# Kernel tuning notes

Hardware: AMD Instinct MI355X
Metric: run time of the kernel (lower is better)

The kernel has to match this reference:

```python
import jax, jax.numpy as jnp
import numpy as np

B = 256   # batch (bs)
N = 6890  # SMPL vertices
J = 24    # joints (root + 23)
NB = 10   # betas
P = 100   # points per foot plane
PARENTS = np.array([-1,0,0,0,1,2,3,4,5,6,7,8,9,9,9,12,13,14,16,17,18,19,20,21], dtype=np.int64)


def setup_inputs() -> dict:
    key = jax.random.key(0)
    ks = jax.random.split(key, 20)
    v_template = jax.random.normal(ks[0], (N, 3), jnp.float32) * 0.3
    shapedirs = jax.random.normal(ks[1], (N, 3, NB), jnp.float32) * 0.01
    Jr = jax.random.uniform(ks[2], (J, N), jnp.float32)
    J_regressor = Jr / Jr.sum(axis=1, keepdims=True)
    lw = jax.random.uniform(ks[3], (N, J), jnp.float32)
    lbs_weights = lw / lw.sum(axis=1, keepdims=True)
    betas = jnp.concatenate([jnp.ones((1, 1), jnp.float32),
                             jax.random.normal(ks[4], (1, NB), jnp.float32) * 0.5], axis=1)
    return dict(
        v_template=v_template, shapedirs=shapedirs, J_regressor=J_regressor,
        lbs_weights=lbs_weights, betas=betas,
        body_pose_wo_foot=jax.random.normal(ks[5], (B, 57), jnp.float32) * 0.2,
        r_back_foot_pose=jax.random.normal(ks[6], (B, 3), jnp.float32) * 0.2,
        r_front_foot_pose=jax.random.normal(ks[7], (B,), jnp.float32) * 0.2,
        l_back_foot_pose=jax.random.normal(ks[8], (B, 3), jnp.float32) * 0.2,
        l_front_foot_pose=jax.random.normal(ks[9], (B,), jnp.float32) * 0.2,
        transl=jax.random.normal(ks[10], (B, 3), jnp.float32) * 0.1,
        global_orient=jax.random.normal(ks[11], (B, 3), jnp.float32) * 0.2,
        init_plane_back_l=jax.random.normal(ks[12], (B, P, 3), jnp.float32) * 0.1,
        init_plane_front_l=jax.random.normal(ks[13], (B, P, 3), jnp.float32) * 0.1,
        init_plane_back_r=jax.random.normal(ks[14], (B, P, 3), jnp.float32) * 0.1,
        init_plane_front_r=jax.random.normal(ks[15], (B, P, 3), jnp.float32) * 0.1,
        parents=jnp.asarray(PARENTS),
        foot_back_l_ids=jax.random.randint(ks[16], (P,), 0, N),
        foot_back_r_ids=jax.random.randint(ks[17], (P,), 0, N),
        foot_front_l_ids=jax.random.randint(ks[18], (P,), 0, N),
        foot_front_r_ids=jax.random.randint(ks[19], (P,), 0, N),
    )


def _rodrigues(rot_vecs):
    # rot_vecs: [M,3] axis-angle -> [M,3,3] rotation matrices (matches SMPL batch_rodrigues)
    angle = jnp.linalg.norm(rot_vecs + 1e-8, axis=1, keepdims=True)  # [M,1]
    rot_dir = rot_vecs / angle
    cos = jnp.cos(angle)[..., None]  # [M,1,1]
    sin = jnp.sin(angle)[..., None]
    rx, ry, rz = rot_dir[:, 0], rot_dir[:, 1], rot_dir[:, 2]
    zeros = jnp.zeros_like(rx)
    K = jnp.stack([zeros, -rz, ry, rz, zeros, -rx, -ry, rx, zeros], axis=1).reshape(-1, 3, 3)
    I = jnp.eye(3, dtype=rot_vecs.dtype)
    return I + sin * K + (1.0 - cos) * jnp.matmul(K, K)


def _forward(v_template, shapedirs, J_regressor, lbs_weights, betas,
             body_pose_wo_foot, r_back_foot_pose, r_front_foot_pose,
             l_back_foot_pose, l_front_foot_pose, transl, global_orient,
             init_plane_back_l, init_plane_front_l, init_plane_back_r, init_plane_front_r,
             ids):
    Bn = body_pose_wo_foot.shape[0]
    dt = v_template.dtype
    # --- update_shape ---
    blend = jnp.einsum('bl,mkl->bmk', betas[:, 1:], shapedirs)            # [1,N,3]
    v_shaped = (v_template[None] + blend) * betas[:, 0][:, None, None]    # [1,N,3]
    J_shaped = jnp.einsum('bik,ji->bjk', v_shaped, J_regressor)           # [1,J,3]
    # --- assemble full pose (foot-joint splicing) ---
    z2 = jnp.zeros((Bn, 2), dt)
    body_pose = jnp.concatenate([
        body_pose_wo_foot[:, :18],              # joints 1..6
        l_back_foot_pose,                       # joint 7
        r_back_foot_pose,                       # joint 8
        body_pose_wo_foot[:, 18:21],            # joint 9
        l_front_foot_pose[:, None], z2,         # joint 10 (x only)
        r_front_foot_pose[:, None], z2,         # joint 11 (x only)
        body_pose_wo_foot[:, 21:]], axis=1)     # joints 12..23
    full_pose = jnp.concatenate([global_orient, body_pose], axis=1)      # [B,72]
    rot = _rodrigues(full_pose.reshape(-1, 3)).reshape(Bn, J, 3, 3)
    # --- batch_rigid_transform ---
    joints = jnp.broadcast_to(J_shaped, (Bn, J, 3))
    rel = jnp.concatenate([joints[:, :1], joints[:, 1:] - joints[:, PARENTS[1:]]], axis=1)
    top = jnp.concatenate([rot, rel[..., None]], axis=-1)                 # [B,J,3,4]
    bottom = jnp.broadcast_to(jnp.array([0., 0., 0., 1.], dt), (Bn, J, 1, 4))
    T_loc = jnp.concatenate([top, bottom], axis=2)                        # [B,J,4,4]
    chain = [T_loc[:, 0]]
    for i in range(1, J):  # fixed 24-joint kinematic chain
        chain.append(chain[int(PARENTS[i])] @ T_loc[:, i])
    transforms = jnp.stack(chain, axis=1)                                 # [B,J,4,4]
    J_transformed = transforms[..., :3, 3]
    init_bone = jnp.einsum('bjmn,bjn->bjm', transforms[..., :3, :3], joints)
    A = transforms.at[..., :3, 3].add(-init_bone)                         # relative transforms
    # --- LBS skinning ---
    T = jnp.einsum('vj,bjmn->bvmn', lbs_weights, A)                       # [B,N,4,4]
    verts = jnp.einsum('bvmn,vn->bvm', T[:, :, :3, :3], v_shaped[0]) + T[:, :, :3, 3] + transl[:, None]
    # --- foot planes ---
    def _plane(idx, init):
        Tp = T[:, idx]                                                    # [B,P,4,4]
        return jnp.einsum('bpmn,bpn->bpm', Tp[:, :, :3, :3], init) + Tp[:, :, :3, 3]
    bl, fl, br, fr = ids
    v_plane = jnp.concatenate([
        _plane(bl, init_plane_back_l), _plane(fl, init_plane_front_l),
        _plane(br, init_plane_back_r), _plane(fr, init_plane_front_r)], axis=1) + transl[:, None]
    return verts, J_transformed, v_plane


def reference(v_template, shapedirs, J_regressor, lbs_weights, betas,
              body_pose_wo_foot, r_back_foot_pose, r_front_foot_pose,
              l_back_foot_pose, l_front_foot_pose, transl, global_orient,
              init_plane_back_l, init_plane_front_l, init_plane_back_r, init_plane_front_r,
              parents, foot_back_l_ids, foot_back_r_ids, foot_front_l_ids, foot_front_r_ids):
    ids = (foot_back_l_ids, foot_front_l_ids, foot_back_r_ids, foot_front_r_ids)
    return _forward(v_template, shapedirs, J_regressor, lbs_weights, betas,
                    body_pose_wo_foot, r_back_foot_pose, r_front_foot_pose,
                    l_back_foot_pose, l_front_foot_pose, transl, global_orient,
                    init_plane_back_l, init_plane_front_l, init_plane_back_r, init_plane_front_r,
                    ids)
```

## Files before the change

kernel.cpp:

```cpp
#include <hip/hip_runtime.h>
#include <stdint.h>

#define NV 6890
#define NJ 24
#define NB_ 256
#define NP 100
#define NBS 8

#define O_VS 0
#define O_JS 20672
#define O_A  20800

#define OUT_JT   5291520
#define OUT_PLN  5309952

__constant__ int c_par[24] = {-1,0,0,0,1,2,3,4,5,6,7,8,9,9,9,12,13,14,16,17,18,19,20,21};

__global__ void k_vshaped(const float* __restrict__ vt, const float* __restrict__ sd,
                          const float* __restrict__ betas, float* __restrict__ ws) {
    int idx = blockIdx.x * 256 + threadIdx.x;
    if (idx >= NV * 3) return;
    float b0 = betas[0];
    float acc = vt[idx];
    const float* row = sd + (size_t)idx * 10;
#pragma unroll
    for (int l = 0; l < 10; ++l) acc += betas[1 + l] * row[l];
    ws[O_VS + idx] = acc * b0;
}

__global__ void k_jshaped(const float* __restrict__ jreg, float* __restrict__ ws) {
    int j = blockIdx.x;
    int tid = threadIdx.x;
    const float* vs = ws + O_VS;
    float s0 = 0.f, s1 = 0.f, s2 = 0.f;
    for (int i = tid; i < NV; i += 256) {
        float w = jreg[(size_t)j * NV + i];
        s0 += w * vs[3 * i + 0];
        s1 += w * vs[3 * i + 1];
        s2 += w * vs[3 * i + 2];
    }
    __shared__ float r0[256], r1[256], r2[256];
    r0[tid] = s0; r1[tid] = s1; r2[tid] = s2;
    __syncthreads();
    for (int off = 128; off > 0; off >>= 1) {
        if (tid < off) { r0[tid] += r0[tid + off]; r1[tid] += r1[tid + off]; r2[tid] += r2[tid + off]; }
        __syncthreads();
    }
    if (tid == 0) {
        ws[O_JS + j * 3 + 0] = r0[0];
        ws[O_JS + j * 3 + 1] = r1[0];
        ws[O_JS + j * 3 + 2] = r2[0];
    }
}

__global__ void k_chain(const float* __restrict__ bpwf, const float* __restrict__ rback,
                        const float* __restrict__ rfront, const float* __restrict__ lback,
                        const float* __restrict__ lfront, const float* __restrict__ gor,
                        float* __restrict__ ws, float* __restrict__ out) {
    int b = blockIdx.x;
    int j = threadIdx.x;
    const float* js = ws + O_JS;
    __shared__ float sT[24][12];
    __shared__ float sJ[24][3];
    if (j < 24) {
        float px, py, pz;
        if (j == 0)      { px = gor[b*3];   py = gor[b*3+1];   pz = gor[b*3+2]; }
        else if (j <= 6) { int o = b*57 + 3*(j-1); px = bpwf[o]; py = bpwf[o+1]; pz = bpwf[o+2]; }
        else if (j == 7) { px = lback[b*3]; py = lback[b*3+1]; pz = lback[b*3+2]; }
        else if (j == 8) { px = rback[b*3]; py = rback[b*3+1]; pz = rback[b*3+2]; }
        else if (j == 9) { int o = b*57 + 18;     px = bpwf[o]; py = bpwf[o+1]; pz = bpwf[o+2]; }
        else if (j == 10){ px = lfront[b];  py = 0.f; pz = 0.f; }
        else if (j == 11){ px = rfront[b];  py = 0.f; pz = 0.f; }
        else             { int o = b*57 + 21 + 3*(j-12); px = bpwf[o]; py = bpwf[o+1]; pz = bpwf[o+2]; }
        float ax = px + 1e-8f, ay = py + 1e-8f, az = pz + 1e-8f;
        float ang = sqrtf(ax*ax + ay*ay + az*az);
        float inv = 1.0f / ang;
        float dx = px * inv, dy = py * inv, dz = pz * inv;
        float c = cosf(ang), s = sinf(ang), t = 1.0f - c;
        sJ[j][0] = js[j*3]; sJ[j][1] = js[j*3+1]; sJ[j][2] = js[j*3+2];
        int p = c_par[j];
        float rx = sJ[j][0], ry = sJ[j][1], rz = sJ[j][2];
        if (p >= 0) { rx -= js[p*3]; ry -= js[p*3+1]; rz -= js[p*3+2]; }
        sT[j][0] = 1.f - t*(dy*dy + dz*dz);
        sT[j][1] = -s*dz + t*dx*dy;
        sT[j][2] =  s*dy + t*dx*dz;
        sT[j][3] = rx;
        sT[j][4] =  s*dz + t*dx*dy;
        sT[j][5] = 1.f - t*(dx*dx + dz*dz);
        sT[j][6] = -s*dx + t*dy*dz;
        sT[j][7] = ry;
        sT[j][8] = -s*dy + t*dx*dz;
        sT[j][9] =  s*dx + t*dy*dz;
        sT[j][10]= 1.f - t*(dx*dx + dy*dy);
        sT[j][11]= rz;
    }
    __syncthreads();
    if (j < 24) {
        int path[12]; int d = 0; int cur = j;
        while (cur >= 0) { path[d++] = cur; cur = c_par[cur]; }
        float g[12];
        int r = path[d - 1];
#pragma unroll
        for (int m = 0; m < 12; ++m) g[m] = sT[r][m];
        for (int i = d - 2; i >= 0; --i) {
            int n = path[i];
            float h[12];
#pragma unroll
            for (int row = 0; row < 3; ++row) {
                float a0 = g[row*4+0], a1 = g[row*4+1], a2 = g[row*4+2], a3 = g[row*4+3];
                h[row*4+0] = a0*sT[n][0] + a1*sT[n][4] + a2*sT[n][8];
                h[row*4+1] = a0*sT[n][1] + a1*sT[n][5] + a2*sT[n][9];
                h[row*4+2] = a0*sT[n][2] + a1*sT[n][6] + a2*sT[n][10];
                h[row*4+3] = a0*sT[n][3] + a1*sT[n][7] + a2*sT[n][11] + a3;
            }
#pragma unroll
            for (int m = 0; m < 12; ++m) g[m] = h[m];
        }
        size_t jo = (size_t)OUT_JT + ((size_t)b * 24 + j) * 3;
        out[jo+0] = g[3]; out[jo+1] = g[7]; out[jo+2] = g[11];
        float jx = sJ[j][0], jy = sJ[j][1], jz = sJ[j][2];
        float* Ab = ws + O_A + ((size_t)b * 24 + j) * 12;
        Ab[0] = g[0]; Ab[1] = g[1]; Ab[2]  = g[2];  Ab[3]  = g[3]  - (g[0]*jx + g[1]*jy + g[2]*jz);
        Ab[4] = g[4]; Ab[5] = g[5]; Ab[6]  = g[6];  Ab[7]  = g[7]  - (g[4]*jx + g[5]*jy + g[6]*jz);
        Ab[8] = g[8]; Ab[9] = g[9]; Ab[10] = g[10]; Ab[11] = g[11] - (g[8]*jx + g[9]*jy + g[10]*jz);
    }
}

__global__ __launch_bounds__(256) void k_lbs(const float* __restrict__ lw,
                                             const float* __restrict__ ws,
                                             const float* __restrict__ transl,
                                             float* __restrict__ out) {
    int v = blockIdx.x * 256 + threadIdx.x;
    if (v >= NV) return;
    float w[24];
    const float* wr = lw + (size_t)v * 24;
#pragma unroll
    for (int j = 0; j < 24; ++j) w[j] = wr[j];
    float vx = ws[O_VS + v*3 + 0], vy = ws[O_VS + v*3 + 1], vz = ws[O_VS + v*3 + 2];
    int b0 = blockIdx.y * NBS;
#pragma unroll 1
    for (int bb = 0; bb < NBS; ++bb) {
        int b = b0 + bb;
        const float* Ab = ws + O_A + (size_t)b * 288;
        float T[12];
#pragma unroll
        for (int m = 0; m < 12; ++m) T[m] = 0.f;
#pragma unroll
        for (int j = 0; j < 24; ++j) {
            float wj = w[j];
#pragma unroll
            for (int m = 0; m < 12; ++m) T[m] += wj * Ab[j*12 + m];
        }
        float ox = T[0]*vx + T[1]*vy + T[2]*vz  + T[3]  + transl[b*3+0];
        float oy = T[4]*vx + T[5]*vy + T[6]*vz  + T[7]  + transl[b*3+1];
        float oz = T[8]*vx + T[9]*vy + T[10]*vz + T[11] + transl[b*3+2];
        size_t o = ((size_t)b * NV + v) * 3;
        out[o+0] = ox; out[o+1] = oy; out[o+2] = oz;
    }
}

__global__ void k_plane(const float* __restrict__ lw, const float* __restrict__ ws,
                        const float* __restrict__ transl,
                        const int* __restrict__ ids_bl, const int* __restrict__ ids_fl,
                        const int* __restrict__ ids_br, const int* __restrict__ ids_fr,
                        const float* __restrict__ ip_bl, const float* __restrict__ ip_fl,
                        const float* __restrict__ ip_br, const float* __restrict__ ip_fr,
                        float* __restrict__ out) {
    int plane = blockIdx.x;
    int b = blockIdx.y;
    int p = threadIdx.x;
    if (p >= NP) return;
    const int* ids   = (plane == 0) ? ids_bl : (plane == 1) ? ids_fl : (plane == 2) ? ids_br : ids_fr;
    const float* ip  = (plane == 0) ? ip_bl  : (plane == 1) ? ip_fl  : (plane == 2) ? ip_br  : ip_fr;
    int vid = ids[p];
    const float* Ab = ws + O_A + (size_t)b * 288;
    const float* w = lw + (size_t)vid * 24;
    float T[12];
#pragma unroll
    for (int m = 0; m < 12; ++m) T[m] = 0.f;
#pragma unroll
    for (int j = 0; j < NJ; ++j) {
        float wj = w[j];
#pragma unroll
        for (int m = 0; m < 12; ++m) T[m] += wj * Ab[j * 12 + m];
    }
    size_t io = ((size_t)b * NP + p) * 3;
    float vx = ip[io+0], vy = ip[io+1], vz = ip[io+2];
    float ox = T[0]*vx + T[1]*vy + T[2]*vz  + T[3]  + transl[b*3+0];
    float oy = T[4]*vx + T[5]*vy + T[6]*vz  + T[7]  + transl[b*3+1];
    float oz = T[8]*vx + T[9]*vy + T[10]*vz + T[11] + transl[b*3+2];
    size_t o = (size_t)OUT_PLN + ((size_t)b * 400 + plane * 100 + p) * 3;
    out[o+0] = ox; out[o+1] = oy; out[o+2] = oz;
}

extern "C" void kernel_launch(void* const* d_in, const int* in_sizes, int n_in,
                              void* d_out, int out_size, void* d_ws, size_t ws_size,
                              hipStream_t stream) {
    const float* vt     = (const float*)d_in[0];
    const float* sd     = (const float*)d_in[1];
    const float* jreg   = (const float*)d_in[2];
    const float* lw     = (const float*)d_in[3];
    const float* betas  = (const float*)d_in[4];
    const float* bpwf   = (const float*)d_in[5];
    const float* rback  = (const float*)d_in[6];
    const float* rfront = (const float*)d_in[7];
    const float* lback  = (const float*)d_in[8];
    const float* lfront = (const float*)d_in[9];
    const float* transl = (const float*)d_in[10];
    const float* gor    = (const float*)d_in[11];
    const float* ip_bl  = (const float*)d_in[12];
    const float* ip_fl  = (const float*)d_in[13];
    const float* ip_br  = (const float*)d_in[14];
    const float* ip_fr  = (const float*)d_in[15];
    const int* ids_bl = (const int*)d_in[17];
    const int* ids_br = (const int*)d_in[18];
    const int* ids_fl = (const int*)d_in[19];
    const int* ids_fr = (const int*)d_in[20];

    float* ws  = (float*)d_ws;
    float* out = (float*)d_out;

    k_vshaped<<<dim3((NV * 3 + 255) / 256), 256, 0, stream>>>(vt, sd, betas, ws);
    k_jshaped<<<dim3(NJ), 256, 0, stream>>>(jreg, ws);
    k_chain  <<<dim3(NB_), 64, 0, stream>>>(bpwf, rback, rfront, lback, lfront, gor, ws, out);
    k_lbs    <<<dim3((NV + 255) / 256, NB_ / NBS), 256, 0, stream>>>(lw, ws, transl, out);
    k_plane  <<<dim3(4, NB_), 128, 0, stream>>>(lw, ws, transl, ids_bl, ids_fl, ids_br, ids_fr,
                                                ip_bl, ip_fl, ip_br, ip_fr, out);
}
```

Baseline: 174.7 us.

## Recast LBS skinning as bf16 MFMA GEMM and fuse launches into three kernels

Skinning is rewritten as one GEMM: a per-vertex matrix of weight times homogeneous rest vertex [6912x96] is multiplied by a per-batch transform matrix [768x96], both in bf16, on MFMA 16x16x32 instructions. The result is staged through shared memory and written out with transl added. The five kernels become three: the shape and joint-regression blocks are merged (joint regression recomputes shaped vertices itself), weight packing is merged with the kinematic chain, and the plane transform is merged into the GEMM kernel. This cuts the scalar FMA work and launch overhead, but bf16 operands lower the precision of the output vertices.

```diff
diff --git a/kernel.cpp b/kernel.cpp
--- a/kernel.cpp
+++ b/kernel.cpp
@@ -5,39 +5,68 @@
 #define NJ 24
 #define NB_ 256
 #define NP 100
-#define NBS 8
+#define MP 6912
+
+typedef unsigned short u16;
+typedef unsigned int u32;
+typedef __attribute__((ext_vector_type(8))) short bf16x8;
+typedef __attribute__((ext_vector_type(4))) float f32x4;
+
+__device__ __forceinline__ u16 f2bf(float f) {
+    u32 u = __float_as_uint(f);
+    u += 0x7FFFu + ((u >> 16) & 1u);
+    return (u16)(u >> 16);
+}
+
+__constant__ int c_par[24] = {-1,0,0,0,1,2,3,4,5,6,7,8,9,9,9,12,13,14,16,17,18,19,20,21};
 
 #define O_VS 0
 #define O_JS 20672
 #define O_A  20800
+#define O_WT 189056
+#define O_AT 852608
 
 #define OUT_JT   5291520
 #define OUT_PLN  5309952
 
-__constant__ int c_par[24] = {-1,0,0,0,1,2,3,4,5,6,7,8,9,9,9,12,13,14,16,17,18,19,20,21};
-
-__global__ void k_vshaped(const float* __restrict__ vt, const float* __restrict__ sd,
-                          const float* __restrict__ betas, float* __restrict__ ws) {
-    int idx = blockIdx.x * 256 + threadIdx.x;
-    if (idx >= NV * 3) return;
+__global__ __launch_bounds__(256) void k_shape(const float* __restrict__ vt,
+                                               const float* __restrict__ sd,
+                                               const float* __restrict__ jreg,
+                                               const float* __restrict__ betas,
+                                               float* __restrict__ ws) {
+    int bx = blockIdx.x;
     float b0 = betas[0];
-    float acc = vt[idx];
-    const float* row = sd + (size_t)idx * 10;
-#pragma unroll
-    for (int l = 0; l < 10; ++l) acc += betas[1 + l] * row[l];
-    ws[O_VS + idx] = acc * b0;
-}
-
-__global__ void k_jshaped(const float* __restrict__ jreg, float* __restrict__ ws) {
-    int j = blockIdx.x;
+    if (bx < 81) {
+        int idx = bx * 256 + threadIdx.x;
+        if (idx < NV * 3) {
+            float acc = vt[idx];
+            const float* row = sd + (size_t)idx * 10;
+#pragma unroll
+            for (int l = 0; l < 10; ++l) acc += betas[1 + l] * row[l];
+            ws[O_VS + idx] = acc * b0;
+        }
+        return;
+    }
+    int j = bx - 81;
     int tid = threadIdx.x;
-    const float* vs = ws + O_VS;
+    float be[10];
+#pragma unroll
+    for (int l = 0; l < 10; ++l) be[l] = betas[1 + l];
     float s0 = 0.f, s1 = 0.f, s2 = 0.f;
     for (int i = tid; i < NV; i += 256) {
         float w = jreg[(size_t)j * NV + i];
-        s0 += w * vs[3 * i + 0];
-        s1 += w * vs[3 * i + 1];
-        s2 += w * vs[3 * i + 2];
+        const float* sr = sd + (size_t)i * 30;
+        const float* vr = vt + (size_t)i * 3;
+        float c0 = vr[0], c1 = vr[1], c2 = vr[2];
+#pragma unroll
+        for (int l = 0; l < 10; ++l) {
+            c0 += be[l] * sr[l];
+            c1 += be[l] * sr[10 + l];
+            c2 += be[l] * sr[20 + l];
+        }
+        s0 += w * (c0 * b0);
+        s1 += w * (c1 * b0);
+        s2 += w * (c2 * b0);
     }
     __shared__ float r0[256], r1[256], r2[256];
     r0[tid] = s0; r1[tid] = s1; r2[tid] = s2;
@@ -53,11 +82,31 @@
     }
 }
 
-__global__ void k_chain(const float* __restrict__ bpwf, const float* __restrict__ rback,
-                        const float* __restrict__ rfront, const float* __restrict__ lback,
-                        const float* __restrict__ lfront, const float* __restrict__ gor,
-                        float* __restrict__ ws, float* __restrict__ out) {
-    int b = blockIdx.x;
+__global__ __launch_bounds__(256) void k_prep(const float* __restrict__ lw,
+                                              const float* __restrict__ bpwf,
+                                              const float* __restrict__ rback,
+                                              const float* __restrict__ rfront,
+                                              const float* __restrict__ lback,
+                                              const float* __restrict__ lfront,
+                                              const float* __restrict__ gor,
+                                              float* __restrict__ ws,
+                                              u16* __restrict__ wsu,
+                                              float* __restrict__ out) {
+    int bx = blockIdx.x;
+    if (bx < 2592) {
+        int idx = bx * 256 + threadIdx.x;
+        int v = idx / 96, k = idx - 96 * v;
+        u16 o = 0;
+        if (v < NV) {
+            int j = k >> 2, n = k & 3;
+            float w = lw[(size_t)v * 24 + j];
+            float h = (n < 3) ? ws[O_VS + v * 3 + n] : 1.0f;
+            o = f2bf(w * h);
+        }
+        wsu[O_WT + idx] = o;
+        return;
+    }
+    int b = bx - 2592;
     int j = threadIdx.x;
     const float* js = ws + O_JS;
     __shared__ float sT[24][12];
@@ -119,78 +168,111 @@
         size_t jo = (size_t)OUT_JT + ((size_t)b * 24 + j) * 3;
         out[jo+0] = g[3]; out[jo+1] = g[7]; out[jo+2] = g[11];
         float jx = sJ[j][0], jy = sJ[j][1], jz = sJ[j][2];
+        float Av[12];
+        Av[0]=g[0]; Av[1]=g[1]; Av[2]=g[2];   Av[3] = g[3]  - (g[0]*jx + g[1]*jy + g[2]*jz);
+        Av[4]=g[4]; Av[5]=g[5]; Av[6]=g[6];   Av[7] = g[7]  - (g[4]*jx + g[5]*jy + g[6]*jz);
+        Av[8]=g[8]; Av[9]=g[9]; Av[10]=g[10]; Av[11]= g[11] - (g[8]*jx + g[9]*jy + g[10]*jz);
         float* Ab = ws + O_A + ((size_t)b * 24 + j) * 12;
-        Ab[0] = g[0]; Ab[1] = g[1]; Ab[2]  = g[2];  Ab[3]  = g[3]  - (g[0]*jx + g[1]*jy + g[2]*jz);
-        Ab[4] = g[4]; Ab[5] = g[5]; Ab[6]  = g[6];  Ab[7]  = g[7]  - (g[4]*jx + g[5]*jy + g[6]*jz);
-        Ab[8] = g[8]; Ab[9] = g[9]; Ab[10] = g[10]; Ab[11] = g[11] - (g[8]*jx + g[9]*jy + g[10]*jz);
-    }
-}
-
-__global__ __launch_bounds__(256) void k_lbs(const float* __restrict__ lw,
-                                             const float* __restrict__ ws,
-                                             const float* __restrict__ transl,
-                                             float* __restrict__ out) {
-    int v = blockIdx.x * 256 + threadIdx.x;
-    if (v >= NV) return;
-    float w[24];
-    const float* wr = lw + (size_t)v * 24;
-#pragma unroll
-    for (int j = 0; j < 24; ++j) w[j] = wr[j];
-    float vx = ws[O_VS + v*3 + 0], vy = ws[O_VS + v*3 + 1], vz = ws[O_VS + v*3 + 2];
-    int b0 = blockIdx.y * NBS;
-#pragma unroll 1
-    for (int bb = 0; bb < NBS; ++bb) {
-        int b = b0 + bb;
+#pragma unroll
+        for (int m = 0; m < 12; ++m) Ab[m] = Av[m];
+        u16* at = wsu + O_AT;
+#pragma unroll
+        for (int m = 0; m < 3; ++m)
+#pragma unroll
+            for (int n = 0; n < 4; ++n)
+                at[(size_t)(b*3 + m) * 96 + j*4 + n] = f2bf(Av[m*4 + n]);
+    }
+}
+
+__global__ __launch_bounds__(256) void k_main(const u16* __restrict__ wsu,
+                                              const float* __restrict__ ws,
+                                              const float* __restrict__ lw,
+                                              const float* __restrict__ transl,
+                                              const int* __restrict__ ids_bl,
+                                              const int* __restrict__ ids_fl,
+                                              const int* __restrict__ ids_br,
+                                              const int* __restrict__ ids_fr,
+                                              const float* __restrict__ ip_bl,
+                                              const float* __restrict__ ip_fl,
+                                              const float* __restrict__ ip_br,
+                                              const float* __restrict__ ip_fr,
+                                              float* __restrict__ out) {
+    if (blockIdx.y < 12) {
+        __shared__ float ltile[64][66];
+        const u16* wt = wsu + O_WT;
+        const u16* at = wsu + O_AT;
+        int lane = threadIdx.x & 63;
+        int wave = threadIdx.x >> 6;
+        int row_in = lane & 15, quad = lane >> 4;
+        int v0 = blockIdx.x * 64 + wave * 16;
+        int c0 = blockIdx.y * 64;
+
+        f32x4 acc0 = {0.f,0.f,0.f,0.f}, acc1 = acc0, acc2 = acc0, acc3 = acc0;
+#pragma unroll
+        for (int kc = 0; kc < 96; kc += 32) {
+            bf16x8 a  = *(const bf16x8*)(wt + (size_t)(v0 + row_in) * 96 + kc + quad * 8);
+            bf16x8 b0 = *(const bf16x8*)(at + (size_t)(c0 +  0 + row_in) * 96 + kc + quad * 8);
+            bf16x8 b1 = *(const bf16x8*)(at + (size_t)(c0 + 16 + row_in) * 96 + kc + quad * 8);
+            bf16x8 b2 = *(const bf16x8*)(at + (size_t)(c0 + 32 + row_in) * 96 + kc + quad * 8);
+            bf16x8 b3 = *(const bf16x8*)(at + (size_t)(c0 + 48 + row_in) * 96 + kc + quad * 8);
+            acc0 = __builtin_amdgcn_mfma_f32_16x16x32_bf16(a, b0, acc0, 0, 0, 0);
+            acc1 = __builtin_amdgcn_mfma_f32_16x16x32_bf16(a, b1, acc1, 0, 0, 0);
+            acc2 = __builtin_amdgcn_mfma_f32_16x16x32_bf16(a, b2, acc2, 0, 0, 0);
+            acc3 = __builtin_amdgcn_mfma_f32_16x16x32_bf16(a, b3, acc3, 0, 0, 0);
+        }
+        int vbase = wave * 16 + quad * 4;
+#pragma unroll
+        for (int s = 0; s < 4; ++s) {
+            f32x4 acc = (s == 0) ? acc0 : (s == 1) ? acc1 : (s == 2) ? acc2 : acc3;
+#pragma unroll
+            for (int r = 0; r < 4; ++r)
+                ltile[vbase + r][s * 16 + row_in] = acc[r];
+        }
+        __syncthreads();
+        int vblk = blockIdx.x * 64;
+        int bstart = c0 / 3;
+        int bend = (c0 + 63) / 3;
+        int tid = threadIdx.x;
+        for (int b = bstart; b <= bend; ++b) {
+            if (tid < 192) {
+                int vl = tid / 3, m = tid - 3 * (tid / 3);
+                int cl = b * 3 + m - c0;
+                int v = vblk + vl;
+                if (cl >= 0 && cl < 64 && v < NV)
+                    out[((size_t)b * NV + v) * 3 + m] = ltile[vl][cl] + transl[b * 3 + m];
+            }
+            if (tid >= 192 && tid < 192 + 64) {
+            }
+        }
+        return;
+    }
+    for (int idx = blockIdx.x * 256 + threadIdx.x; idx < NB_ * 400; idx += 108 * 256) {
+        int b = idx / 400;
+        int rr = idx - 400 * b;
+        int plane = rr / 100;
+        int p = rr - 100 * plane;
+        const int* ids   = (plane == 0) ? ids_bl : (plane == 1) ? ids_fl : (plane == 2) ? ids_br : ids_fr;
+        const float* ip  = (plane == 0) ? ip_bl  : (plane == 1) ? ip_fl  : (plane == 2) ? ip_br  : ip_fr;
+        int vid = ids[p];
         const float* Ab = ws + O_A + (size_t)b * 288;
+        const float* w = lw + (size_t)vid * 24;
         float T[12];
 #pragma unroll
         for (int m = 0; m < 12; ++m) T[m] = 0.f;
 #pragma unroll
-        for (int j = 0; j < 24; ++j) {
+        for (int j = 0; j < NJ; ++j) {
             float wj = w[j];
 #pragma unroll
-            for (int m = 0; m < 12; ++m) T[m] += wj * Ab[j*12 + m];
-        }
+            for (int m = 0; m < 12; ++m) T[m] += wj * Ab[j * 12 + m];
+        }
+        size_t io = ((size_t)b * NP + p) * 3;
+        float vx = ip[io+0], vy = ip[io+1], vz = ip[io+2];
         float ox = T[0]*vx + T[1]*vy + T[2]*vz  + T[3]  + transl[b*3+0];
         float oy = T[4]*vx + T[5]*vy + T[6]*vz  + T[7]  + transl[b*3+1];
         float oz = T[8]*vx + T[9]*vy + T[10]*vz + T[11] + transl[b*3+2];
-        size_t o = ((size_t)b * NV + v) * 3;
+        size_t o = (size_t)OUT_PLN + (size_t)idx * 3;
         out[o+0] = ox; out[o+1] = oy; out[o+2] = oz;
     }
-}
-
-__global__ void k_plane(const float* __restrict__ lw, const float* __restrict__ ws,
-                        const float* __restrict__ transl,
-                        const int* __restrict__ ids_bl, const int* __restrict__ ids_fl,
-                        const int* __restrict__ ids_br, const int* __restrict__ ids_fr,
-                        const float* __restrict__ ip_bl, const float* __restrict__ ip_fl,
-                        const float* __restrict__ ip_br, const float* __restrict__ ip_fr,
-                        float* __restrict__ out) {
-    int plane = blockIdx.x;
-    int b = blockIdx.y;
-    int p = threadIdx.x;
-    if (p >= NP) return;
-    const int* ids   = (plane == 0) ? ids_bl : (plane == 1) ? ids_fl : (plane == 2) ? ids_br : ids_fr;
-    const float* ip  = (plane == 0) ? ip_bl  : (plane == 1) ? ip_fl  : (plane == 2) ? ip_br  : ip_fr;
-    int vid = ids[p];
-    const float* Ab = ws + O_A + (size_t)b * 288;
-    const float* w = lw + (size_t)vid * 24;
-    float T[12];
-#pragma unroll
-    for (int m = 0; m < 12; ++m) T[m] = 0.f;
-#pragma unroll
-    for (int j = 0; j < NJ; ++j) {
-        float wj = w[j];
-#pragma unroll
-        for (int m = 0; m < 12; ++m) T[m] += wj * Ab[j * 12 + m];
-    }
-    size_t io = ((size_t)b * NP + p) * 3;
-    float vx = ip[io+0], vy = ip[io+1], vz = ip[io+2];
-    float ox = T[0]*vx + T[1]*vy + T[2]*vz  + T[3]  + transl[b*3+0];
-    float oy = T[4]*vx + T[5]*vy + T[6]*vz  + T[7]  + transl[b*3+1];
-    float oz = T[8]*vx + T[9]*vy + T[10]*vz + T[11] + transl[b*3+2];
-    size_t o = (size_t)OUT_PLN + ((size_t)b * 400 + plane * 100 + p) * 3;
-    out[o+0] = ox; out[o+1] = oy; out[o+2] = oz;
 }
 
 extern "C" void kernel_launch(void* const* d_in, const int* in_sizes, int n_in,
@@ -218,12 +300,13 @@
     const int* ids_fr = (const int*)d_in[20];
 
     float* ws  = (float*)d_ws;
+    u16*   wsu = (u16*)d_ws;
     float* out = (float*)d_out;
 
-    k_vshaped<<<dim3((NV * 3 + 255) / 256), 256, 0, stream>>>(vt, sd, betas, ws);
-    k_jshaped<<<dim3(NJ), 256, 0, stream>>>(jreg, ws);
-    k_chain  <<<dim3(NB_), 64, 0, stream>>>(bpwf, rback, rfront, lback, lfront, gor, ws, out);
-    k_lbs    <<<dim3((NV + 255) / 256, NB_ / NBS), 256, 0, stream>>>(lw, ws, transl, out);
-    k_plane  <<<dim3(4, NB_), 128, 0, stream>>>(lw, ws, transl, ids_bl, ids_fl, ids_br, ids_fr,
-                                                ip_bl, ip_fl, ip_br, ip_fr, out);
-}
+    k_shape<<<dim3(81 + 24), 256, 0, stream>>>(vt, sd, jreg, betas, ws);
+    k_prep <<<dim3(2592 + 256), 256, 0, stream>>>(lw, bpwf, rback, rfront, lback, lfront, gor,
+                                                  ws, wsu, out);
+    k_main <<<dim3(108, 13), 256, 0, stream>>>(wsu, ws, lw, transl,
+                                               ids_bl, ids_fl, ids_br, ids_fr,
+                                               ip_bl, ip_fl, ip_br, ip_fr, out);
+}
```

Result: faster. 147.8 us (-15.4%).
